# Kernel tuning notes

Hardware: AMD Instinct MI355X
Metric: run time of the kernel (lower is better)

## Reference

```python
import jax, jax.numpy as jnp
import numpy as np

N_NODES = 50000
N_EDGES = 600000
N_GRAPHS = 1024
H = 128
VOCAB = 32
NC = 2
BN_EPS = 1e-5


def setup_inputs() -> dict:
    key = jax.random.key(0)
    ks = jax.random.split(key, 16)
    rn = lambda k, s, sc=0.05: jax.random.normal(k, s, jnp.float32) * sc
    inp = {}
    inp["node_feat"] = jax.random.randint(ks[0], (N_NODES,), 0, VOCAB, dtype=jnp.int32)
    inp["edge_src"] = jax.random.randint(ks[1], (N_EDGES,), 0, N_NODES, dtype=jnp.int32)
    inp["edge_dst"] = jax.random.randint(ks[2], (N_EDGES,), 0, N_NODES, dtype=jnp.int32)
    inp["graph_ids"] = jnp.sort(jax.random.randint(ks[3], (N_NODES,), 0, N_GRAPHS, dtype=jnp.int32))
    inp["emb"] = rn(ks[4], (VOCAB, H))
    inp["W1"] = rn(ks[5], (H, H)); inp["b1"] = jnp.zeros((H,), jnp.float32)
    inp["W2"] = rn(ks[6], (H, H)); inp["b2"] = jnp.zeros((H,), jnp.float32)
    inp["e1_w"] = rn(ks[7], (H, H));   inp["e1_b"] = jnp.zeros((H,), jnp.float32)
    inp["e2_w"] = rn(ks[8], (H, H));   inp["e2_b"] = jnp.zeros((H,), jnp.float32)
    inp["e3_w"] = rn(ks[9], (H, 64));  inp["e3_b"] = jnp.zeros((64,), jnp.float32)
    inp["e4_w"] = rn(ks[10], (64, 32)); inp["e4_b"] = jnp.zeros((32,), jnp.float32)
    inp["e5_w"] = rn(ks[11], (32, NC)); inp["e5_b"] = jnp.zeros((NC,), jnp.float32)
    inp["bn0_g"] = jnp.ones((H,), jnp.float32); inp["bn0_b"] = jnp.zeros((H,), jnp.float32)
    inp["bn1_g"] = jnp.ones((H,), jnp.float32); inp["bn1_b"] = jnp.zeros((H,), jnp.float32)
    return inp


def reference(node_feat, edge_src, edge_dst, graph_ids,
              emb, W1, b1, W2, b2,
              e1_w, e1_b, e2_w, e2_b, e3_w, e3_b, e4_w, e4_b, e5_w, e5_b,
              bn0_g, bn0_b, bn1_g, bn1_b):
    ones_e = jnp.ones((N_EDGES,), jnp.float32)
    out_deg = jax.ops.segment_sum(ones_e, edge_src, num_segments=N_NODES)
    in_deg = jax.ops.segment_sum(ones_e, edge_dst, num_segments=N_NODES)
    # DGL GraphConv norm='both': D_out^{-1/2} pre-scale, D_in^{-1/2} post-scale (deg clamped to 1)
    oi = jax.lax.rsqrt(jnp.maximum(out_deg, 1.0))  # [N]
    ii = jax.lax.rsqrt(jnp.maximum(in_deg, 1.0))   # [N]

    def gconv(h, W, b):
        m = (h * oi[:, None])[edge_src]                                   # [E,H] gather
        agg = jax.ops.segment_sum(m, edge_dst, num_segments=N_NODES)      # [N,H] scatter-add
        return (agg * ii[:, None]) @ W + b

    h = emb[node_feat]                       # [N,H] embedding lookup
    h = jax.nn.relu(gconv(h, W1, b1))
    h = jax.nn.relu(gconv(h, W2, b2))

    # dgl.mean_nodes: per-graph mean over nodes
    cnt = jax.ops.segment_sum(jnp.ones((N_NODES,), jnp.float32), graph_ids, num_segments=N_GRAPHS)
    hg = jax.ops.segment_sum(h, graph_ids, num_segments=N_GRAPHS) / jnp.maximum(cnt, 1.0)[:, None]

    def bn(x, g, b):  # BatchNorm1d, training-mode batch stats (biased var)
        mu = x.mean(0)
        var = x.var(0)
        return (x - mu) * jax.lax.rsqrt(var + BN_EPS) * g + b

    def lrelu(x, s):
        return jnp.where(x >= 0, x, s * x)

    h1 = lrelu(bn(hg @ e1_w + e1_b, bn0_g, bn0_b), 0.05)
    h2 = lrelu(bn(h1 @ e2_w + e2_b, bn1_g, bn1_b), 0.05)
    h3 = lrelu(h2 @ e3_w + e3_b, 0.1)
    h4 = lrelu(h3 @ e4_w + e4_b, 0.1)
    y = h4 @ e5_w + e5_b                      # [G, NC]
    return jax.nn.log_softmax(y, axis=1)
```

## Files before the change

### kernel.cpp

```cpp
#include <hip/hip_runtime.h>
#include <hip/hip_bf16.h>
#include <math.h>

#define N_NODES 50000
#define N_EDGES 600000
#define N_GRAPHS 1024
#define H 128
#define VOCAB 32
#define BN_EPS 1e-5f
#define SCAN_BLOCKS ((N_NODES + 255) / 256)
#define H1_NODES 64
#define EB ((N_EDGES + 255) / 256)
#define GM_NODES 16
#define SROW 136
#define ZERO_BYTES ((size_t)N_NODES * 4 + (size_t)N_NODES * VOCAB * 4)
#define ZERO_N16 ((int)(ZERO_BYTES / 16))

typedef short bf8_t __attribute__((ext_vector_type(8)));
typedef float f4_t __attribute__((ext_vector_type(4)));

__global__ void k_zero(uint4* __restrict__ p, int n16) {
    int i = blockIdx.x * blockDim.x + threadIdx.x;
    if (i < n16) p[i] = uint4{0u, 0u, 0u, 0u};
}

__global__ void k_count_prep(const int* __restrict__ src, int* __restrict__ cntO,
                             const float* __restrict__ emb, const float* __restrict__ W1,
                             float* __restrict__ emb1,
                             const float* __restrict__ W2, __hip_bfloat16* __restrict__ w2t) {
    int b = blockIdx.x;
    int t = threadIdx.x;
    if (b < EB) {
        int i = b * 256 + t;
        if (i < N_EDGES) atomicAdd(&cntO[src[i]], 1);
    } else if (b < EB + 32) {
        if (t < 128) {
            int v = b - EB;
            float acc = 0.f;
            for (int k = 0; k < H; ++k) acc += emb[v * H + k] * W1[k * H + t];
            emb1[v * H + t] = acc;
        }
    } else {
        if (t < 128) {
            int k = b - EB - 32;
            w2t[(size_t)t * H + k] = __float2bfloat16(W2[(size_t)k * H + t]);
        }
    }
}

__global__ void k_hist32(const int* __restrict__ src, const int* __restrict__ dst,
                         const int* __restrict__ feat, const int* __restrict__ cntO,
                         unsigned* __restrict__ wc,
                         unsigned char* __restrict__ rank8, int E) {
    int i = blockIdx.x * blockDim.x + threadIdx.x;
    if (i >= E) return;
    int s = src[i], d = dst[i], v = feat[s];
    float o = rsqrtf(fmaxf((float)cntO[s], 1.f));
    unsigned q = __float2uint_rn(o * 1048576.0f);
    unsigned old = atomicAdd(&wc[(size_t)d * VOCAB + v], (1u << 27) | q);
    rank8[i] = (unsigned char)(old >> 27);
}

__global__ void k_nodebins(const unsigned* __restrict__ wc,
                           int* __restrict__ cntI, unsigned char* __restrict__ binbase,
                           int* __restrict__ bsum, int n) {
    __shared__ int scnt[256];
    int t = threadIdx.x;
    int wave = t >> 6, lane = t & 63;
    int sub = lane >> 5;
    int l32 = lane & 31;
    int nodeBase = blockIdx.x * 256;
#pragma unroll 4
    for (int it = 0; it < 32; ++it) {
        int local = wave * 64 + it * 2 + sub;
        int node = nodeBase + local;
        int c = 0;
        if (node < n && l32 < VOCAB)
            c = (int)(wc[(size_t)node * VOCAB + l32] >> 27);
        int inc = c;
#pragma unroll
        for (int off = 1; off < VOCAB; off <<= 1) {
            int u = __shfl_up(inc, off, 32);
            if (l32 >= off) inc += u;
        }
        if (node < n && l32 < VOCAB)
            binbase[(size_t)node * VOCAB + l32] = (unsigned char)(inc - c);
        if (l32 == VOCAB - 1) scnt[local] = (node < n) ? inc : 0;
    }
    __syncthreads();
    int node = nodeBase + t;
    if (node < n) cntI[node] = scnt[t];
    __shared__ int red[256];
    red[t] = scnt[t];
    __syncthreads();
    for (int off = 128; off > 0; off >>= 1) {
        if (t < off) red[t] += red[t + off];
        __syncthreads();
    }
    if (t == 0) bsum[blockIdx.x] = red[0];
}

__global__ void k_scatterscan(const int* __restrict__ cntI, const int* __restrict__ bsum,
                              int* __restrict__ row_ptr, float* __restrict__ ii,
                              int n, int nb) {
    __shared__ int sb[256];
    __shared__ int sh[256];
    int t = threadIdx.x;
    int bv = (t < nb) ? bsum[t] : 0;
    sb[t] = bv;
    __syncthreads();
    for (int off = 1; off < 256; off <<= 1) {
        int u = (t >= off) ? sb[t - off] : 0;
        __syncthreads();
        sb[t] += u;
        __syncthreads();
    }
    int blockoff = (blockIdx.x == 0) ? 0 : sb[blockIdx.x - 1];
    int i = blockIdx.x * 256 + t;
    int v = (i < n) ? cntI[i] : 0;
    sh[t] = v;
    __syncthreads();
    for (int off = 1; off < 256; off <<= 1) {
        int u = (t >= off) ? sh[t - off] : 0;
        __syncthreads();
        sh[t] += u;
        __syncthreads();
    }
    if (i < n) {
        row_ptr[i] = blockoff + sh[t] - v;
        ii[i] = rsqrtf(fmaxf((float)v, 1.f));
    }
    if (blockIdx.x == 0 && t == 0) row_ptr[n] = sb[nb - 1];
}

#define H1_BLOCKS ((N_NODES + H1_NODES - 1) / H1_NODES)
__global__ void k_fill_h1(const int* __restrict__ src, const int* __restrict__ dst,
                          const int* __restrict__ feat, const int* __restrict__ row_ptr,
                          const unsigned char* __restrict__ binbase,
                          const unsigned char* __restrict__ rank8,
                          int* __restrict__ col,
                          const unsigned* __restrict__ wc,
                          const float* __restrict__ emb1,
                          const float* __restrict__ ii, const int* __restrict__ cntO,
                          const float* __restrict__ b1, __hip_bfloat16* __restrict__ h1) {
    __shared__ float wl[H1_NODES * VOCAB];
    __shared__ float sii[H1_NODES], soi[H1_NODES];
    int tid = threadIdx.x;
    if (blockIdx.x < EB) {
        int i = blockIdx.x * 256 + tid;
        if (i < N_EDGES) {
            int s = src[i], d = dst[i], v = feat[s];
            int slot = row_ptr[d] + (int)binbase[(size_t)d * VOCAB + v] + (int)rank8[i];
            col[slot] = s;
        }
        return;
    }
    int hb = blockIdx.x - EB;
    int j = tid & 127;
    int g = tid >> 7;
    float ev[VOCAB];
#pragma unroll
    for (int v = 0; v < VOCAB; ++v) ev[v] = emb1[v * H + j];
    float bj = b1[j];

    int node0 = hb * H1_NODES;
    int nn = min(H1_NODES, N_NODES - node0);
    const unsigned* wsrc = wc + (size_t)node0 * VOCAB;
    for (int i = tid; i < nn * VOCAB; i += 256) {
        unsigned p = wsrc[i];
        wl[i] = (float)(p & 0x07FFFFFFu) * (1.0f / 1048576.0f);
    }
    for (int i = tid; i < nn; i += 256) {
        sii[i] = ii[node0 + i];
        soi[i] = rsqrtf(fmaxf((float)cntO[node0 + i], 1.f));
    }
    __syncthreads();

    int rbeg = g * 32;
    int rend = min(rbeg + 32, nn);
    for (int r = rbeg; r < rend; ++r) {
        const float4* wr = (const float4*)(wl + r * VOCAB);
        float acc = 0.f;
#pragma unroll
        for (int q = 0; q < VOCAB / 4; ++q) {
            float4 w4 = wr[q];
            acc += w4.x * ev[4 * q] + w4.y * ev[4 * q + 1]
                 + w4.z * ev[4 * q + 2] + w4.w * ev[4 * q + 3];
        }
        float val = fmaxf(acc * sii[r] + bj, 0.f);
        h1[(size_t)(node0 + r) * H + j] = __float2bfloat16(val * soi[r]);
    }
}

__global__ __launch_bounds__(256) void k_gather_mfma(
        const __hip_bfloat16* __restrict__ h,
        const int* __restrict__ row_ptr, const int* __restrict__ col,
        const __hip_bfloat16* __restrict__ WT,
        const float* __restrict__ ii, const float* __restrict__ b,
        __hip_bfloat16* __restrict__ outp, int n) {
    __shared__ __hip_bfloat16 sA[GM_NODES * SROW];
    int tid = threadIdx.x;
    int wave = tid >> 6;
    int lane = tid & 63;
    int l16 = lane & 15;
    int sub = lane >> 4;
    int co = l16 * 8;
    int base = blockIdx.x * GM_NODES;

    int local = wave * 4 + sub;
    int node = base + local;
    float a0 = 0.f, a1 = 0.f, a2 = 0.f, a3 = 0.f;
    float a4 = 0.f, a5 = 0.f, a6 = 0.f, a7 = 0.f;
    if (node < n) {
        int beg = row_ptr[node];
        int end = row_ptr[node + 1];
        int e = beg;
        for (; e + 16 <= end; e += 16) {
            int s[16];
            uint4 v[16];
#pragma unroll
            for (int k = 0; k < 16; ++k) s[k] = col[e + k];
#pragma unroll
            for (int k = 0; k < 16; ++k)
                v[k] = *(const uint4*)(h + (size_t)s[k] * H + co);
#pragma unroll
            for (int k = 0; k < 16; ++k) {
                float2 f0 = __bfloat1622float2(*(__hip_bfloat162*)&v[k].x);
                float2 f1 = __bfloat1622float2(*(__hip_bfloat162*)&v[k].y);
                float2 f2 = __bfloat1622float2(*(__hip_bfloat162*)&v[k].z);
                float2 f3 = __bfloat1622float2(*(__hip_bfloat162*)&v[k].w);
                a0 += f0.x; a1 += f0.y; a2 += f1.x; a3 += f1.y;
                a4 += f2.x; a5 += f2.y; a6 += f3.x; a7 += f3.y;
            }
        }
        if (e < end) {
            int s[16];
            uint4 v[16];
#pragma unroll
            for (int k = 0; k < 16; ++k) s[k] = col[(e + k < end) ? e + k : e];
#pragma unroll
            for (int k = 0; k < 16; ++k)
                v[k] = *(const uint4*)(h + (size_t)s[k] * H + co);
#pragma unroll
            for (int k = 0; k < 16; ++k) {
                float mk = (e + k < end) ? 1.f : 0.f;
                float2 f0 = __bfloat1622float2(*(__hip_bfloat162*)&v[k].x);
                float2 f1 = __bfloat1622float2(*(__hip_bfloat162*)&v[k].y);
                float2 f2 = __bfloat1622float2(*(__hip_bfloat162*)&v[k].z);
                float2 f3 = __bfloat1622float2(*(__hip_bfloat162*)&v[k].w);
                a0 += mk * f0.x; a1 += mk * f0.y; a2 += mk * f1.x; a3 += mk * f1.y;
                a4 += mk * f2.x; a5 += mk * f2.y; a6 += mk * f3.x; a7 += mk * f3.y;
            }
        }
    }
    __hip_bfloat162 o0 = __float22bfloat162_rn(make_float2(a0, a1));
    __hip_bfloat162 o1 = __float22bfloat162_rn(make_float2(a2, a3));
    __hip_bfloat162 o2 = __float22bfloat162_rn(make_float2(a4, a5));
    __hip_bfloat162 o3 = __float22bfloat162_rn(make_float2(a6, a7));
    uint4 ov;
    ov.x = *(unsigned*)&o0; ov.y = *(unsigned*)&o1;
    ov.z = *(unsigned*)&o2; ov.w = *(unsigned*)&o3;
    *(uint4*)(&sA[local * SROW + co]) = ov;
    __syncthreads();

    int rl = l16;
    int kg = sub;
    f4_t acc[2];
    acc[0] = f4_t{0.f, 0.f, 0.f, 0.f};
    acc[1] = f4_t{0.f, 0.f, 0.f, 0.f};
    const __hip_bfloat16* arow = &sA[rl * SROW + kg * 8];
#pragma unroll
    for (int ks = 0; ks < 4; ++ks) {
        bf8_t a = *(const bf8_t*)(arow + ks * 32);
#pragma unroll
        for (int t = 0; t < 2; ++t) {
            int ct = wave * 2 + t;
            bf8_t bf = *(const bf8_t*)(WT + (size_t)(ct * 16 + rl) * H + ks * 32 + kg * 8);
            acc[t] = __builtin_amdgcn_mfma_f32_16x16x32_bf16(a, bf, acc[t], 0, 0, 0);
        }
    }
    int rbase = base + kg * 4;
#pragma unroll
    for (int r = 0; r < 4; ++r) {
        int nd = rbase + r;
        if (nd < n) {
            float s = ii[nd];
#pragma unroll
            for (int t = 0; t < 2; ++t) {
                int c = (wave * 2 + t) * 16 + rl;
                float v = acc[t][r] * s + b[c];
                outp[(size_t)nd * H + c] = __float2bfloat16(fmaxf(v, 0.f));
            }
        }
    }
}

__global__ void k_poolmlp1(const __hip_bfloat16* __restrict__ h, const int* __restrict__ gid,
                           const float* __restrict__ e1w, const float* __restrict__ e1b,
                           float* __restrict__ t1, int n) {
    __shared__ int bnd[2];
    __shared__ float row[128];
    int g = blockIdx.x, t = threadIdx.x;
    if (t == 0) {
        int lo = 0, hi = n;
        while (lo < hi) { int m = (lo + hi) >> 1; if (gid[m] < g) lo = m + 1; else hi = m; }
        bnd[0] = lo;
        int lo2 = lo, hi2 = n;
        while (lo2 < hi2) { int m = (lo2 + hi2) >> 1; if (gid[m] < g + 1) lo2 = m + 1; else hi2 = m; }
        bnd[1] = lo2;
    }
    __syncthreads();
    int beg = bnd[0], end = bnd[1];
    float s = 0.f;
    for (int i = beg; i < end; ++i) s += __bfloat162float(h[(size_t)i * H + t]);
    row[t] = s / fmaxf((float)(end - beg), 1.f);
    __syncthreads();
    float acc = e1b[t];
    for (int k = 0; k < H; ++k) acc += row[k] * e1w[k * H + t];
    t1[g * H + t] = acc;
}

__global__ void k_bnstat(const float* __restrict__ x, float* __restrict__ stats, int G) {
    int c = blockIdx.x;
    float s = 0.f, s2 = 0.f;
    for (int g = threadIdx.x; g < G; g += blockDim.x) {
        float v = x[g * H + c];
        s += v; s2 += v * v;
    }
    __shared__ float rs[256], rs2[256];
    rs[threadIdx.x] = s; rs2[threadIdx.x] = s2;
    __syncthreads();
    for (int off = 128; off > 0; off >>= 1) {
        if (threadIdx.x < off) { rs[threadIdx.x] += rs[threadIdx.x + off]; rs2[threadIdx.x] += rs2[threadIdx.x + off]; }
        __syncthreads();
    }
    if (threadIdx.x == 0) {
        float mu = rs[0] / G;
        stats[c] = mu;
        stats[H + c] = rs2[0] / G - mu * mu;
    }
}

__global__ void k_mlp2bn(const float* __restrict__ t1, const float* __restrict__ stats,
                         const float* __restrict__ gam, const float* __restrict__ bet,
                         const float* __restrict__ W, const float* __restrict__ bias,
                         float* __restrict__ t2) {
    __shared__ float x[128];
    int g = blockIdx.x, t = threadIdx.x;
    float v = t1[g * H + t];
    v = (v - stats[t]) * rsqrtf(stats[H + t] + BN_EPS) * gam[t] + bet[t];
    x[t] = (v >= 0.f) ? v : 0.05f * v;
    __syncthreads();
    float acc = bias[t];
    for (int k = 0; k < H; ++k) acc += x[k] * W[k * H + t];
    t2[g * H + t] = acc;
}

__global__ void k_head(const float* __restrict__ t2, const float* __restrict__ stats,
                       const float* __restrict__ gam, const float* __restrict__ bet,
                       const float* __restrict__ e3w, const float* __restrict__ e3b,
                       const float* __restrict__ e4w, const float* __restrict__ e4b,
                       const float* __restrict__ e5w, const float* __restrict__ e5b,
                       float* __restrict__ out) {
    __shared__ float x[128], h3[64], h4[32];
    int g = blockIdx.x, t = threadIdx.x;
    float v = t2[g * H + t];
    v = (v - stats[t]) * rsqrtf(stats[H + t] + BN_EPS) * gam[t] + bet[t];
    x[t] = (v >= 0.f) ? v : 0.05f * v;
    __syncthreads();
    if (t < 64) {
        float a = e3b[t];
        for (int k = 0; k < 128; ++k) a += x[k] * e3w[k * 64 + t];
        h3[t] = (a >= 0.f) ? a : 0.1f * a;
    }
    __syncthreads();
    if (t < 32) {
        float a = e4b[t];
        for (int k = 0; k < 64; ++k) a += h3[k] * e4w[k * 32 + t];
        h4[t] = (a >= 0.f) ? a : 0.1f * a;
    }
    __syncthreads();
    if (t == 0) {
        float y0 = e5b[0], y1 = e5b[1];
        for (int k = 0; k < 32; ++k) {
            y0 += h4[k] * e5w[2 * k];
            y1 += h4[k] * e5w[2 * k + 1];
        }
        float m = fmaxf(y0, y1);
        float l = m + logf(expf(y0 - m) + expf(y1 - m));
        out[2 * g] = y0 - l;
        out[2 * g + 1] = y1 - l;
    }
}

extern "C" void kernel_launch(void* const* d_in, const int* in_sizes, int n_in,
                              void* d_out, int out_size, void* d_ws, size_t ws_size,
                              hipStream_t stream) {
    const int*   node_feat = (const int*)d_in[0];
    const int*   edge_src  = (const int*)d_in[1];
    const int*   edge_dst  = (const int*)d_in[2];
    const int*   graph_ids = (const int*)d_in[3];
    const float* emb  = (const float*)d_in[4];
    const float* W1   = (const float*)d_in[5];
    const float* b1   = (const float*)d_in[6];
    const float* W2   = (const float*)d_in[7];
    const float* b2   = (const float*)d_in[8];
    const float* e1_w = (const float*)d_in[9];
    const float* e1_b = (const float*)d_in[10];
    const float* e2_w = (const float*)d_in[11];
    const float* e2_b = (const float*)d_in[12];
    const float* e3_w = (const float*)d_in[13];
    const float* e3_b = (const float*)d_in[14];
    const float* e4_w = (const float*)d_in[15];
    const float* e4_b = (const float*)d_in[16];
    const float* e5_w = (const float*)d_in[17];
    const float* e5_b = (const float*)d_in[18];
    const float* bn0_g = (const float*)d_in[19];
    const float* bn0_b = (const float*)d_in[20];
    const float* bn1_g = (const float*)d_in[21];
    const float* bn1_b = (const float*)d_in[22];
    float* out = (float*)d_out;

    float* ws = (float*)d_ws;
    float* bufA = ws;
    __hip_bfloat16* h2bf = (__hip_bfloat16*)bufA;
    __hip_bfloat16* h1bf = (__hip_bfloat16*)(bufA + (size_t)N_NODES * H);
    int*   cntO = (int*)(h1bf + (size_t)N_NODES * H);
    unsigned* wc = (unsigned*)(cntO + N_NODES);
    float* ii   = (float*)(wc + (size_t)N_NODES * VOCAB);
    int*   cntI = (int*)(ii + N_NODES);
    int*   row_ptr = cntI + N_NODES;
    int*   col  = row_ptr + 50048;
    unsigned char* binbase = (unsigned char*)(col + N_EDGES);
    unsigned char* rank8   = binbase + (size_t)N_NODES * VOCAB;
    float* t1   = (float*)(rank8 + ((N_EDGES + 63) & ~63));
    float* t2   = t1 + N_GRAPHS * H;
    float* stats = t2 + N_GRAPHS * H;
    int*   bsum  = (int*)(stats + 4 * H);
    float* emb1  = (float*)(bsum + 256);
    __hip_bfloat16* w2t = (__hip_bfloat16*)(emb1 + VOCAB * H);

    k_zero<<<(ZERO_N16 + 255) / 256, 256, 0, stream>>>((uint4*)cntO, ZERO_N16);

    k_count_prep<<<EB + 160, 256, 0, stream>>>(edge_src, cntO, emb, W1, emb1, W2, w2t);
    k_hist32<<<EB, 256, 0, stream>>>(edge_src, edge_dst, node_feat, cntO, wc, rank8, N_EDGES);
    k_nodebins<<<SCAN_BLOCKS, 256, 0, stream>>>(wc, cntI, binbase, bsum, N_NODES);
    k_scatterscan<<<SCAN_BLOCKS, 256, 0, stream>>>(cntI, bsum, row_ptr, ii, N_NODES, SCAN_BLOCKS);
    k_fill_h1<<<EB + H1_BLOCKS, 256, 0, stream>>>(edge_src, edge_dst, node_feat, row_ptr,
                                                  binbase, rank8, col,
                                                  wc, emb1, ii, cntO, b1, h1bf);

    k_gather_mfma<<<(N_NODES + GM_NODES - 1) / GM_NODES, 256, 0, stream>>>(
        h1bf, row_ptr, col, w2t, ii, b2, h2bf, N_NODES);

    k_poolmlp1<<<N_GRAPHS, 128, 0, stream>>>(h2bf, graph_ids, e1_w, e1_b, t1, N_NODES);
    k_bnstat<<<H, 256, 0, stream>>>(t1, stats, N_GRAPHS);
    k_mlp2bn<<<N_GRAPHS, 128, 0, stream>>>(t1, stats, bn0_g, bn0_b, e2_w, e2_b, t2);
    k_bnstat<<<H, 256, 0, stream>>>(t2, stats + 2 * H, N_GRAPHS);
    k_head<<<N_GRAPHS, 128, 0, stream>>>(t2, stats + 2 * H, bn1_g, bn1_b,
                                         e3_w, e3_b, e4_w, e4_b, e5_w, e5_b, out);
}
```

Baseline: 203.6 us.

## Merge histogram into edge-count pass and build layer-1 weights from CSR in LDS

Folds the per-(dst,vocab) histogram atomic into the first edge pass, so a separate edge kernel and the dependency on finished out-degree counts go away. The layer-1 weighted sums are no longer accumulated as packed fixed-point global atomics. Instead k_h1 walks each block's CSR segment, finds each edge's row by binary search over row_ptr in LDS, and accumulates the quantized out-norm weights with LDS atomics. col now packs the vocab id into the upper 16 bits, and the gather kernel masks it off. The cost is an extra kernel launch, since fill and h1 are split, plus the binary-search work per edge.

```diff
diff --git a/kernel.cpp b/kernel.cpp
--- a/kernel.cpp
+++ b/kernel.cpp
@@ -10,6 +10,7 @@
 #define BN_EPS 1e-5f
 #define SCAN_BLOCKS ((N_NODES + 255) / 256)
 #define H1_NODES 64
+#define H1_BLOCKS ((N_NODES + H1_NODES - 1) / H1_NODES)
 #define EB ((N_EDGES + 255) / 256)
 #define GM_NODES 16
 #define SROW 136
@@ -24,15 +25,23 @@
     if (i < n16) p[i] = uint4{0u, 0u, 0u, 0u};
 }
 
-__global__ void k_count_prep(const int* __restrict__ src, int* __restrict__ cntO,
-                             const float* __restrict__ emb, const float* __restrict__ W1,
-                             float* __restrict__ emb1,
-                             const float* __restrict__ W2, __hip_bfloat16* __restrict__ w2t) {
+__global__ void k_edge(const int* __restrict__ src, const int* __restrict__ dst,
+                       const int* __restrict__ feat,
+                       int* __restrict__ cntO, unsigned* __restrict__ cnt32,
+                       unsigned char* __restrict__ rank8,
+                       const float* __restrict__ emb, const float* __restrict__ W1,
+                       float* __restrict__ emb1,
+                       const float* __restrict__ W2, __hip_bfloat16* __restrict__ w2t) {
     int b = blockIdx.x;
     int t = threadIdx.x;
     if (b < EB) {
         int i = b * 256 + t;
-        if (i < N_EDGES) atomicAdd(&cntO[src[i]], 1);
+        if (i < N_EDGES) {
+            int s = src[i];
+            atomicAdd(&cntO[s], 1);
+            unsigned old = atomicAdd(&cnt32[(size_t)dst[i] * VOCAB + feat[s]], 1u);
+            rank8[i] = (unsigned char)old;
+        }
     } else if (b < EB + 32) {
         if (t < 128) {
             int v = b - EB;
@@ -48,20 +57,7 @@
     }
 }
 
-__global__ void k_hist32(const int* __restrict__ src, const int* __restrict__ dst,
-                         const int* __restrict__ feat, const int* __restrict__ cntO,
-                         unsigned* __restrict__ wc,
-                         unsigned char* __restrict__ rank8, int E) {
-    int i = blockIdx.x * blockDim.x + threadIdx.x;
-    if (i >= E) return;
-    int s = src[i], d = dst[i], v = feat[s];
-    float o = rsqrtf(fmaxf((float)cntO[s], 1.f));
-    unsigned q = __float2uint_rn(o * 1048576.0f);
-    unsigned old = atomicAdd(&wc[(size_t)d * VOCAB + v], (1u << 27) | q);
-    rank8[i] = (unsigned char)(old >> 27);
-}
-
-__global__ void k_nodebins(const unsigned* __restrict__ wc,
+__global__ void k_nodebins(const unsigned* __restrict__ cnt32,
                            int* __restrict__ cntI, unsigned char* __restrict__ binbase,
                            int* __restrict__ bsum, int n) {
     __shared__ int scnt[256];
@@ -76,7 +72,7 @@
         int node = nodeBase + local;
         int c = 0;
         if (node < n && l32 < VOCAB)
-            c = (int)(wc[(size_t)node * VOCAB + l32] >> 27);
+            c = (int)cnt32[(size_t)node * VOCAB + l32];
         int inc = c;
 #pragma unroll
         for (int off = 1; off < VOCAB; off <<= 1) {
@@ -133,48 +129,61 @@
     if (blockIdx.x == 0 && t == 0) row_ptr[n] = sb[nb - 1];
 }
 
-#define H1_BLOCKS ((N_NODES + H1_NODES - 1) / H1_NODES)
-__global__ void k_fill_h1(const int* __restrict__ src, const int* __restrict__ dst,
-                          const int* __restrict__ feat, const int* __restrict__ row_ptr,
-                          const unsigned char* __restrict__ binbase,
-                          const unsigned char* __restrict__ rank8,
-                          int* __restrict__ col,
-                          const unsigned* __restrict__ wc,
-                          const float* __restrict__ emb1,
-                          const float* __restrict__ ii, const int* __restrict__ cntO,
-                          const float* __restrict__ b1, __hip_bfloat16* __restrict__ h1) {
-    __shared__ float wl[H1_NODES * VOCAB];
+__global__ void k_fill(const int* __restrict__ src, const int* __restrict__ dst,
+                       const int* __restrict__ feat, const int* __restrict__ row_ptr,
+                       const unsigned char* __restrict__ binbase,
+                       const unsigned char* __restrict__ rank8,
+                       int* __restrict__ col, int E) {
+    int i = blockIdx.x * blockDim.x + threadIdx.x;
+    if (i >= E) return;
+    int s = src[i], d = dst[i], v = feat[s];
+    int slot = row_ptr[d] + (int)binbase[(size_t)d * VOCAB + v] + (int)rank8[i];
+    col[slot] = s | (v << 16);
+}
+
+__global__ void k_h1(const int* __restrict__ row_ptr, const int* __restrict__ col,
+                     const int* __restrict__ cntO,
+                     const float* __restrict__ emb1, const float* __restrict__ ii,
+                     const float* __restrict__ b1, __hip_bfloat16* __restrict__ h1, int n) {
+    __shared__ int srp[H1_NODES + 1];
+    __shared__ unsigned wlq[H1_NODES * VOCAB];
     __shared__ float sii[H1_NODES], soi[H1_NODES];
     int tid = threadIdx.x;
-    if (blockIdx.x < EB) {
-        int i = blockIdx.x * 256 + tid;
-        if (i < N_EDGES) {
-            int s = src[i], d = dst[i], v = feat[s];
-            int slot = row_ptr[d] + (int)binbase[(size_t)d * VOCAB + v] + (int)rank8[i];
-            col[slot] = s;
-        }
-        return;
-    }
-    int hb = blockIdx.x - EB;
+    int node0 = blockIdx.x * H1_NODES;
+    int nn = min(H1_NODES, n - node0);
+
+    for (int i = tid; i <= nn; i += 256) srp[i] = row_ptr[node0 + i];
+    for (int i = tid; i < nn * VOCAB; i += 256) wlq[i] = 0u;
+    for (int i = tid; i < nn; i += 256) {
+        sii[i] = ii[node0 + i];
+        soi[i] = rsqrtf(fmaxf((float)cntO[node0 + i], 1.f));
+    }
+    __syncthreads();
+
+    int ebeg = srp[0], eend = srp[nn];
+    for (int e = ebeg + tid; e < eend; e += 256) {
+        int c = col[e];
+        int s = c & 0xFFFF;
+        int v = c >> 16;
+        float o = rsqrtf(fmaxf((float)cntO[s], 1.f));
+        unsigned q = __float2uint_rn(o * 1048576.0f);
+        int lo = 0, hi = nn;
+        while (lo + 1 < hi) { int m = (lo + hi) >> 1; if (srp[m] <= e) lo = m; else hi = m; }
+        atomicAdd(&wlq[lo * VOCAB + v], q);
+    }
+    __syncthreads();
+
+    float* wl = (float*)wlq;
+    for (int i = tid; i < nn * VOCAB; i += 256)
+        wl[i] = (float)wlq[i] * (1.0f / 1048576.0f);
+    __syncthreads();
+
     int j = tid & 127;
     int g = tid >> 7;
     float ev[VOCAB];
 #pragma unroll
     for (int v = 0; v < VOCAB; ++v) ev[v] = emb1[v * H + j];
     float bj = b1[j];
-
-    int node0 = hb * H1_NODES;
-    int nn = min(H1_NODES, N_NODES - node0);
-    const unsigned* wsrc = wc + (size_t)node0 * VOCAB;
-    for (int i = tid; i < nn * VOCAB; i += 256) {
-        unsigned p = wsrc[i];
-        wl[i] = (float)(p & 0x07FFFFFFu) * (1.0f / 1048576.0f);
-    }
-    for (int i = tid; i < nn; i += 256) {
-        sii[i] = ii[node0 + i];
-        soi[i] = rsqrtf(fmaxf((float)cntO[node0 + i], 1.f));
-    }
-    __syncthreads();
 
     int rbeg = g * 32;
     int rend = min(rbeg + 32, nn);
@@ -219,7 +228,7 @@
             int s[16];
             uint4 v[16];
 #pragma unroll
-            for (int k = 0; k < 16; ++k) s[k] = col[e + k];
+            for (int k = 0; k < 16; ++k) s[k] = col[e + k] & 0xFFFF;
 #pragma unroll
             for (int k = 0; k < 16; ++k)
                 v[k] = *(const uint4*)(h + (size_t)s[k] * H + co);
@@ -237,7 +246,7 @@
             int s[16];
             uint4 v[16];
 #pragma unroll
-            for (int k = 0; k < 16; ++k) s[k] = col[(e + k < end) ? e + k : e];
+            for (int k = 0; k < 16; ++k) s[k] = col[(e + k < end) ? e + k : e] & 0xFFFF;
 #pragma unroll
             for (int k = 0; k < 16; ++k)
                 v[k] = *(const uint4*)(h + (size_t)s[k] * H + co);
@@ -426,8 +435,8 @@
     __hip_bfloat16* h2bf = (__hip_bfloat16*)bufA;
     __hip_bfloat16* h1bf = (__hip_bfloat16*)(bufA + (size_t)N_NODES * H);
     int*   cntO = (int*)(h1bf + (size_t)N_NODES * H);
-    unsigned* wc = (unsigned*)(cntO + N_NODES);
-    float* ii   = (float*)(wc + (size_t)N_NODES * VOCAB);
+    unsigned* cnt32 = (unsigned*)(cntO + N_NODES);
+    float* ii   = (float*)(cnt32 + (size_t)N_NODES * VOCAB);
     int*   cntI = (int*)(ii + N_NODES);
     int*   row_ptr = cntI + N_NODES;
     int*   col  = row_ptr + 50048;
@@ -442,13 +451,14 @@
 
     k_zero<<<(ZERO_N16 + 255) / 256, 256, 0, stream>>>((uint4*)cntO, ZERO_N16);
 
-    k_count_prep<<<EB + 160, 256, 0, stream>>>(edge_src, cntO, emb, W1, emb1, W2, w2t);
-    k_hist32<<<EB, 256, 0, stream>>>(edge_src, edge_dst, node_feat, cntO, wc, rank8, N_EDGES);
-    k_nodebins<<<SCAN_BLOCKS, 256, 0, stream>>>(wc, cntI, binbase, bsum, N_NODES);
+    k_edge<<<EB + 160, 256, 0, stream>>>(edge_src, edge_dst, node_feat, cntO, cnt32, rank8,
+                                         emb, W1, emb1, W2, w2t);
+    k_nodebins<<<SCAN_BLOCKS, 256, 0, stream>>>(cnt32, cntI, binbase, bsum, N_NODES);
     k_scatterscan<<<SCAN_BLOCKS, 256, 0, stream>>>(cntI, bsum, row_ptr, ii, N_NODES, SCAN_BLOCKS);
-    k_fill_h1<<<EB + H1_BLOCKS, 256, 0, stream>>>(edge_src, edge_dst, node_feat, row_ptr,
-                                                  binbase, rank8, col,
-                                                  wc, emb1, ii, cntO, b1, h1bf);
+    k_fill<<<EB, 256, 0, stream>>>(edge_src, edge_dst, node_feat, row_ptr, binbase, rank8,
+                                   col, N_EDGES);
+
+    k_h1<<<H1_BLOCKS, 256, 0, stream>>>(row_ptr, col, cntO, emb1, ii, b1, h1bf, N_NODES);
 
     k_gather_mfma<<<(N_NODES + GM_NODES - 1) / GM_NODES, 256, 0, stream>>>(
         h1bf, row_ptr, col, w2t, ii, b2, h2bf, N_NODES);
```

New measurement: 204.2 us. Within noise of the previous version (+0.3%).

## Fuse pooling, BN stats and MLP head into one cooperative kernel

Applied to the files above, without the earlier changes.

Replaces the five tail launches (pool+MLP1, two BN-stat reductions, MLP2, head) with a single cooperative kernel of 1024 blocks. Grid-wide syncs separate the stages, and the first 128 blocks compute the per-channel batch statistics in between. This is meant to remove the launch gaps and drain/refill of several small kernels. The cost is the overhead of grid.sync, and the launch depends on all 1024 blocks of 128 threads being co-resident, which a GPU with many CUs should allow.

```diff
diff --git a/kernel.cpp b/kernel.cpp
--- a/kernel.cpp
+++ b/kernel.cpp
@@ -1,6 +1,9 @@
 #include <hip/hip_runtime.h>
 #include <hip/hip_bf16.h>
+#include <hip/hip_cooperative_groups.h>
 #include <math.h>
+
+namespace cg = cooperative_groups;
 
 #define N_NODES 50000
 #define N_EDGES 600000
@@ -10,6 +13,7 @@
 #define BN_EPS 1e-5f
 #define SCAN_BLOCKS ((N_NODES + 255) / 256)
 #define H1_NODES 64
+#define H1_BLOCKS ((N_NODES + H1_NODES - 1) / H1_NODES)
 #define EB ((N_EDGES + 255) / 256)
 #define GM_NODES 16
 #define SROW 136
@@ -133,7 +137,6 @@
     if (blockIdx.x == 0 && t == 0) row_ptr[n] = sb[nb - 1];
 }
 
-#define H1_BLOCKS ((N_NODES + H1_NODES - 1) / H1_NODES)
 __global__ void k_fill_h1(const int* __restrict__ src, const int* __restrict__ dst,
                           const int* __restrict__ feat, const int* __restrict__ row_ptr,
                           const unsigned char* __restrict__ binbase,
@@ -295,12 +298,24 @@
     }
 }
 
-__global__ void k_poolmlp1(const __hip_bfloat16* __restrict__ h, const int* __restrict__ gid,
-                           const float* __restrict__ e1w, const float* __restrict__ e1b,
-                           float* __restrict__ t1, int n) {
+__global__ void k_headall(const __hip_bfloat16* __restrict__ h, const int* __restrict__ gid,
+                          const float* __restrict__ e1w, const float* __restrict__ e1b,
+                          const float* __restrict__ bn0g, const float* __restrict__ bn0b,
+                          const float* __restrict__ e2w, const float* __restrict__ e2b,
+                          const float* __restrict__ bn1g, const float* __restrict__ bn1b,
+                          const float* __restrict__ e3w, const float* __restrict__ e3b,
+                          const float* __restrict__ e4w, const float* __restrict__ e4b,
+                          const float* __restrict__ e5w, const float* __restrict__ e5b,
+                          float* __restrict__ t1, float* __restrict__ t2,
+                          float* __restrict__ stats, float* __restrict__ out, int n) {
+    cg::grid_group grid = cg::this_grid();
     __shared__ int bnd[2];
     __shared__ float row[128];
+    __shared__ float x[128];
+    __shared__ float rs[128], rs2[128];
+    __shared__ float h3[64], h4[32];
     int g = blockIdx.x, t = threadIdx.x;
+
     if (t == 0) {
         int lo = 0, hi = n;
         while (lo < hi) { int m = (lo + hi) >> 1; if (gid[m] < g) lo = m + 1; else hi = m; }
@@ -315,58 +330,71 @@
     for (int i = beg; i < end; ++i) s += __bfloat162float(h[(size_t)i * H + t]);
     row[t] = s / fmaxf((float)(end - beg), 1.f);
     __syncthreads();
-    float acc = e1b[t];
-    for (int k = 0; k < H; ++k) acc += row[k] * e1w[k * H + t];
-    t1[g * H + t] = acc;
-}
-
-__global__ void k_bnstat(const float* __restrict__ x, float* __restrict__ stats, int G) {
-    int c = blockIdx.x;
-    float s = 0.f, s2 = 0.f;
-    for (int g = threadIdx.x; g < G; g += blockDim.x) {
-        float v = x[g * H + c];
-        s += v; s2 += v * v;
-    }
-    __shared__ float rs[256], rs2[256];
-    rs[threadIdx.x] = s; rs2[threadIdx.x] = s2;
-    __syncthreads();
-    for (int off = 128; off > 0; off >>= 1) {
-        if (threadIdx.x < off) { rs[threadIdx.x] += rs[threadIdx.x + off]; rs2[threadIdx.x] += rs2[threadIdx.x + off]; }
-        __syncthreads();
-    }
-    if (threadIdx.x == 0) {
-        float mu = rs[0] / G;
-        stats[c] = mu;
-        stats[H + c] = rs2[0] / G - mu * mu;
-    }
-}
-
-__global__ void k_mlp2bn(const float* __restrict__ t1, const float* __restrict__ stats,
-                         const float* __restrict__ gam, const float* __restrict__ bet,
-                         const float* __restrict__ W, const float* __restrict__ bias,
-                         float* __restrict__ t2) {
-    __shared__ float x[128];
-    int g = blockIdx.x, t = threadIdx.x;
-    float v = t1[g * H + t];
-    v = (v - stats[t]) * rsqrtf(stats[H + t] + BN_EPS) * gam[t] + bet[t];
-    x[t] = (v >= 0.f) ? v : 0.05f * v;
-    __syncthreads();
-    float acc = bias[t];
-    for (int k = 0; k < H; ++k) acc += x[k] * W[k * H + t];
-    t2[g * H + t] = acc;
-}
-
-__global__ void k_head(const float* __restrict__ t2, const float* __restrict__ stats,
-                       const float* __restrict__ gam, const float* __restrict__ bet,
-                       const float* __restrict__ e3w, const float* __restrict__ e3b,
-                       const float* __restrict__ e4w, const float* __restrict__ e4b,
-                       const float* __restrict__ e5w, const float* __restrict__ e5b,
-                       float* __restrict__ out) {
-    __shared__ float x[128], h3[64], h4[32];
-    int g = blockIdx.x, t = threadIdx.x;
-    float v = t2[g * H + t];
-    v = (v - stats[t]) * rsqrtf(stats[H + t] + BN_EPS) * gam[t] + bet[t];
-    x[t] = (v >= 0.f) ? v : 0.05f * v;
+    {
+        float acc = e1b[t];
+        for (int k = 0; k < H; ++k) acc += row[k] * e1w[k * H + t];
+        t1[g * H + t] = acc;
+    }
+    grid.sync();
+
+    if (g < H) {
+        float ss = 0.f, ss2 = 0.f;
+        for (int r = t; r < N_GRAPHS; r += 128) {
+            float v = t1[r * H + g];
+            ss += v; ss2 += v * v;
+        }
+        rs[t] = ss; rs2[t] = ss2;
+        __syncthreads();
+        for (int off = 64; off > 0; off >>= 1) {
+            if (t < off) { rs[t] += rs[t + off]; rs2[t] += rs2[t + off]; }
+            __syncthreads();
+        }
+        if (t == 0) {
+            float mu = rs[0] / N_GRAPHS;
+            stats[g] = mu;
+            stats[H + g] = rs2[0] / N_GRAPHS - mu * mu;
+        }
+    }
+    grid.sync();
+
+    {
+        float v = t1[g * H + t];
+        v = (v - stats[t]) * rsqrtf(stats[H + t] + BN_EPS) * bn0g[t] + bn0b[t];
+        x[t] = (v >= 0.f) ? v : 0.05f * v;
+    }
+    __syncthreads();
+    {
+        float acc = e2b[t];
+        for (int k = 0; k < H; ++k) acc += x[k] * e2w[k * H + t];
+        t2[g * H + t] = acc;
+    }
+    grid.sync();
+
+    if (g < H) {
+        float ss = 0.f, ss2 = 0.f;
+        for (int r = t; r < N_GRAPHS; r += 128) {
+            float v = t2[r * H + g];
+            ss += v; ss2 += v * v;
+        }
+        rs[t] = ss; rs2[t] = ss2;
+        __syncthreads();
+        for (int off = 64; off > 0; off >>= 1) {
+            if (t < off) { rs[t] += rs[t + off]; rs2[t] += rs2[t + off]; }
+            __syncthreads();
+        }
+        if (t == 0) {
+            float mu = rs[0] / N_GRAPHS;
+            stats[2 * H + g] = mu;
+            stats[3 * H + g] = rs2[0] / N_GRAPHS - mu * mu;
+        }
+    }
+    grid.sync();
+
+    {
+        float v = t2[g * H + t];
+        v = (v - stats[2 * H + t]) * rsqrtf(stats[3 * H + t] + BN_EPS) * bn1g[t] + bn1b[t];
+        x[t] = (v >= 0.f) ? v : 0.05f * v;
+    }
     __syncthreads();
     if (t < 64) {
         float a = e3b[t];
@@ -453,10 +481,12 @@
     k_gather_mfma<<<(N_NODES + GM_NODES - 1) / GM_NODES, 256, 0, stream>>>(
         h1bf, row_ptr, col, w2t, ii, b2, h2bf, N_NODES);
 
-    k_poolmlp1<<<N_GRAPHS, 128, 0, stream>>>(h2bf, graph_ids, e1_w, e1_b, t1, N_NODES);
-    k_bnstat<<<H, 256, 0, stream>>>(t1, stats, N_GRAPHS);
-    k_mlp2bn<<<N_GRAPHS, 128, 0, stream>>>(t1, stats, bn0_g, bn0_b, e2_w, e2_b, t2);
-    k_bnstat<<<H, 256, 0, stream>>>(t2, stats + 2 * H, N_GRAPHS);
-    k_head<<<N_GRAPHS, 128, 0, stream>>>(t2, stats + 2 * H, bn1_g, bn1_b,
-                                         e3_w, e3_b, e4_w, e4_b, e5_w, e5_b, out);
-}
+    int nNodes = N_NODES;
+    void* args[] = {(void*)&h2bf, (void*)&graph_ids,
+                    (void*)&e1_w, (void*)&e1_b, (void*)&bn0_g, (void*)&bn0_b,
+                    (void*)&e2_w, (void*)&e2_b, (void*)&bn1_g, (void*)&bn1_b,
+                    (void*)&e3_w, (void*)&e3_b, (void*)&e4_w, (void*)&e4_b,
+                    (void*)&e5_w, (void*)&e5_b,
+                    (void*)&t1, (void*)&t2, (void*)&stats, (void*)&out, (void*)&nNodes};
+    hipLaunchCooperativeKernel((void*)k_headall, dim3(N_GRAPHS), dim3(128), args, 0, stream);
+}
```

Measured after the change: 654.8 us. +221.7%, slower.
